# Kernel optimization log

Hardware: AMD Instinct MI355X
Metric: run time of the kernel (lower is better)

Reference implementation:

```python
import jax, jax.numpy as jnp
import numpy as np

B, T, D = 8, 4096, 1024

def setup_inputs() -> dict:
    key = jax.random.key(0)
    k1, k2, k3, k4, k5 = jax.random.split(key, 5)
    s = 1.0 / np.sqrt(D)
    return {
        "seq": jax.random.normal(k1, (B, T, D), dtype=jnp.float32),
        "W_delta": jax.random.uniform(k2, (D, D), jnp.float32, -s, s),
        "b_delta": jax.random.uniform(k3, (D,), jnp.float32, -s, s),
        "W_value": jax.random.uniform(k4, (D, D), jnp.float32, -s, s),
        "b_value": jax.random.uniform(k5, (D,), jnp.float32, -s, s),
    }

def reference(seq, W_delta, b_delta, W_value, b_value):
    # delta = sigmoid(seq @ W_delta^T + b_delta); value = seq @ W_value^T + b_value
    delta = jax.nn.sigmoid(jnp.einsum("btd,ed->bte", seq, W_delta) + b_delta)
    value = jnp.einsum("btd,ed->bte", seq, W_value) + b_value
    # gated linear recurrence: state_t = (1-delta_t)*state_{t-1} + delta_t*value_t
    def step(state, dv):
        d, v = dv  # each [B, D]
        state = (1.0 - d) * state + d * v
        return state, state
    init = jnp.zeros((seq.shape[0], seq.shape[-1]), dtype=seq.dtype)
    # time-major for scan
    _, out = jax.lax.scan(step, init, (delta.transpose(1, 0, 2), value.transpose(1, 0, 2)))
    return out.transpose(1, 0, 2)  # [B, T, D]
```

## Files before the change

kernel.cpp:

```cpp
#include <hip/hip_runtime.h>
#include <hip/hip_bf16.h>


typedef _Float16 f16;
typedef _Float16 f16x8 __attribute__((ext_vector_type(8)));
typedef float    f32x4 __attribute__((ext_vector_type(4)));

#define NB  8
#define NT  4096
#define ND  1024
#define NM  (NB*NT)
#define KK  1024

#define CT  64
#define NCH (NT/CT)

#define OFF_AP     0UL
#define OFF_BP     67108864UL
#define OFF_VALUE  71303168UL
#define OFF_AARR   205520896UL
#define OFF_SARR   207618048UL
#define OFF_SIN    209715200UL

#define GLOAD_LDS16(gp, lp)                                                          \
  __builtin_amdgcn_global_load_lds(                                                  \
      (const __attribute__((address_space(1))) void*)(gp),                           \
      (__attribute__((address_space(3))) void*)(lp), 16, 0, 0)

#define MEMFENCE asm volatile("" ::: "memory")
#define BARRIER() do { MEMFENCE; __builtin_amdgcn_s_barrier(); MEMFENCE; } while (0)
#define WAITV2() asm volatile("s_waitcnt vmcnt(2)" ::: "memory")
#define WAITV0() asm volatile("s_waitcnt vmcnt(0)" ::: "memory")

__global__ void k_convert_seq(const float* __restrict__ src, f16* __restrict__ Ap) {
  const long n8 = (long)NM * ND / 8;
  long i = (long)blockIdx.x * blockDim.x + threadIdx.x;
  const long stride = (long)gridDim.x * blockDim.x;
  for (; i < n8; i += stride) {
    const float4 v0 = *(const float4*)(src + i * 8);
    const float4 v1 = *(const float4*)(src + i * 8 + 4);
    f16x8 h;
    h[0] = (f16)v0.x; h[1] = (f16)v0.y; h[2] = (f16)v0.z; h[3] = (f16)v0.w;
    h[4] = (f16)v1.x; h[5] = (f16)v1.y; h[6] = (f16)v1.z; h[7] = (f16)v1.w;
    *((f16x8*)Ap + i) = h;
  }
}

__global__ void k_convert_w(const float* __restrict__ Wd, const float* __restrict__ Wv,
                            f16* __restrict__ Bp) {
  const long i = (long)blockIdx.x * blockDim.x + threadIdx.x;
  const int n = (int)(i >> 7);
  const int k8 = ((int)i & 127) * 8;
  const float* row = (n < ND) ? (Wd + (long)n * ND) : (Wv + (long)(n - ND) * ND);
  const float4 v0 = *(const float4*)(row + k8);
  const float4 v1 = *(const float4*)(row + k8 + 4);
  f16x8 h;
  h[0] = (f16)v0.x; h[1] = (f16)v0.y; h[2] = (f16)v0.z; h[3] = (f16)v0.w;
  h[4] = (f16)v1.x; h[5] = (f16)v1.y; h[6] = (f16)v1.z; h[7] = (f16)v1.w;
  *(f16x8*)(Bp + (long)n * ND + k8) = h;
}

#define LDS_A(c) ((c) * 65536)
#define LDS_B(c) ((c) * 65536 + 32768)

__global__ __launch_bounds__(512, 2) void k_gemm(
    const f16* __restrict__ Ap, const f16* __restrict__ Bp,
    const float* __restrict__ bd, const float* __restrict__ bv,
    float* __restrict__ dOut, float* __restrict__ vOut) {
  __shared__ char smem[131072];

  const int t = threadIdx.x;
  const int w = t >> 6, lane = t & 63;
  const int wr = w >> 2, wc = w & 3;
  const int l15 = lane & 15, l4 = lane >> 4;

  const int bid = blockIdx.x;
  const int sw = (bid & 7) * 128 + (bid >> 3);
  const int bm = sw >> 3, bn = sw & 7;
  const long m0 = (long)bm * 256;
  const int n0 = bn * 256;

  f32x4 acc[8][4] = {};

  const int rl0 = t >> 3;
  const int rl1 = 64 + (t >> 3);
  const int c16_0 = (t & 7) ^ (rl0 & 7);
  const int c16_1 = (t & 7) ^ (rl1 & 7);

  auto stageA = [&](int kt, int h, int c) {
    const f16* s0 = Ap + (m0 + h * 128 + rl0) * (long)KK + kt * 64 + c16_0 * 8;
    const f16* s1 = Ap + (m0 + h * 128 + rl1) * (long)KK + kt * 64 + c16_1 * 8;
    char* base = smem + LDS_A(c) + h * 16384 + w * 1024;
    GLOAD_LDS16(s0, base);
    GLOAD_LDS16(s1, base + 8192);
  };
  auto stageB = [&](int kt, int h, int c) {
    const f16* s0 = Bp + (long)(n0 + h * 128 + rl0) * ND + kt * 64 + c16_0 * 8;
    const f16* s1 = Bp + (long)(n0 + h * 128 + rl1) * ND + kt * 64 + c16_1 * 8;
    char* base = smem + LDS_B(c) + h * 16384 + w * 1024;
    GLOAD_LDS16(s0, base);
    GLOAD_LDS16(s1, base + 8192);
  };

  f16x8 aF[8], bF[2];
  auto readA = [&](int c, int k) {
#pragma unroll
    for (int mf = 0; mf < 8; ++mf) {
      const int row = wr * 128 + mf * 16 + l15;
      const int c16 = (k * 4 + l4) ^ (row & 7);
      aF[mf] = *(const f16x8*)(smem + LDS_A(c) + row * 128 + c16 * 16);
    }
  };
  auto readB = [&](int c, int k, int nh) {
#pragma unroll
    for (int nfl = 0; nfl < 2; ++nfl) {
      const int row = nh * 128 + wc * 32 + nfl * 16 + l15;
      const int c16 = (k * 4 + l4) ^ (row & 7);
      bF[nfl] = *(const f16x8*)(smem + LDS_B(c) + row * 128 + c16 * 16);
    }
  };
  auto mfmaQ = [&](int nh) {
    __builtin_amdgcn_s_setprio(1);
#pragma unroll
    for (int mf = 0; mf < 8; ++mf)
#pragma unroll
      for (int nfl = 0; nfl < 2; ++nfl)
        acc[mf][nh * 2 + nfl] = __builtin_amdgcn_mfma_f32_16x16x32_f16(
            bF[nfl], aF[mf], acc[mf][nh * 2 + nfl], 0, 0, 0);
    __builtin_amdgcn_s_setprio(0);
  };

  auto tile = [&](int c, int ktNext, bool pf) {
    if (pf) stageA(ktNext, 0, c ^ 1);
    readA(c, 0); readB(c, 0, 0);
    BARRIER();
    mfmaQ(0);
    if (pf) { WAITV2(); } else { WAITV0(); }
    BARRIER();
    if (pf) stageA(ktNext, 1, c ^ 1);
    readB(c, 0, 1);
    BARRIER();
    mfmaQ(1);
    BARRIER();
    if (pf) stageB(ktNext, 0, c ^ 1);
    readA(c, 1); readB(c, 1, 0);
    BARRIER();
    mfmaQ(0);
    BARRIER();
    if (pf) stageB(ktNext, 1, c ^ 1);
    readB(c, 1, 1);
    BARRIER();
    mfmaQ(1);
    if (pf) { WAITV2(); } else { WAITV0(); }
    BARRIER();
  };

  stageA(0, 0, 0); stageA(0, 1, 0); stageB(0, 0, 0); stageB(0, 1, 0);
  WAITV2();
  BARRIER();

  for (int i = 0; i < 8; ++i) {
    tile(0, 2 * i + 1, true);
    tile(1, 2 * i + 2, i < 7);
  }

  const bool isDelta = (n0 < ND);
#pragma unroll
  for (int nf = 0; nf < 4; ++nf) {
    const int nb = n0 + (nf >> 1) * 128 + wc * 32 + (nf & 1) * 16 + l4 * 4;
    const float4 bias = *(const float4*)(isDelta ? (bd + nb) : (bv + (nb - ND)));
#pragma unroll
    for (int mf = 0; mf < 8; ++mf) {
      const long m = m0 + wr * 128 + mf * 16 + l15;
      f32x4 x = acc[mf][nf];
      x[0] += bias.x; x[1] += bias.y; x[2] += bias.z; x[3] += bias.w;
      if (isDelta) {
#pragma unroll
        for (int r = 0; r < 4; ++r) x[r] = 1.0f / (1.0f + __expf(-x[r]));
        *(f32x4*)(dOut + m * ND + nb) = x;
      } else {
        *(f32x4*)(vOut + m * ND + (nb - ND)) = x;
      }
    }
  }
}

__global__ void k_scan_local(const float* __restrict__ delta, const float* __restrict__ value,
                             float* __restrict__ Aarr, float* __restrict__ Sarr) {
  const int bid = blockIdx.x;
  const int c = bid & 63, b = bid >> 6;
  const int d = threadIdx.x * 4;
  const long base = ((long)b * NT + (long)c * CT) * ND + d;
  float4 a = make_float4(1.f, 1.f, 1.f, 1.f);
  float4 s = make_float4(0.f, 0.f, 0.f, 0.f);
#pragma unroll 4
  for (int tt = 0; tt < CT; ++tt) {
    const float4 dl = *(const float4*)(delta + base + (long)tt * ND);
    const float4 v  = *(const float4*)(value + base + (long)tt * ND);
    const float o0 = 1.0f - dl.x, o1 = 1.0f - dl.y, o2 = 1.0f - dl.z, o3 = 1.0f - dl.w;
    a.x *= o0; a.y *= o1; a.z *= o2; a.w *= o3;
    s.x = o0 * s.x + dl.x * v.x;
    s.y = o1 * s.y + dl.y * v.y;
    s.z = o2 * s.z + dl.z * v.z;
    s.w = o3 * s.w + dl.w * v.w;
  }
  const long o = (long)(b * NCH + c) * ND + d;
  *(float4*)(Aarr + o) = a;
  *(float4*)(Sarr + o) = s;
}

__global__ void k_scan_prefix(const float* __restrict__ Aarr, const float* __restrict__ Sarr,
                              float* __restrict__ Sin) {
  const int tid = blockIdx.x * blockDim.x + threadIdx.x;
  const int b = tid >> 8, d = (tid & 255) * 4;
  float4 st = make_float4(0.f, 0.f, 0.f, 0.f);
  for (int c = 0; c < NCH; ++c) {
    const long idx = (long)(b * NCH + c) * ND + d;
    *(float4*)(Sin + idx) = st;
    const float4 a = *(const float4*)(Aarr + idx);
    const float4 s = *(const float4*)(Sarr + idx);
    st.x = a.x * st.x + s.x;
    st.y = a.y * st.y + s.y;
    st.z = a.z * st.z + s.z;
    st.w = a.w * st.w + s.w;
  }
}

__global__ void k_scan_apply(const float* __restrict__ value, const float* __restrict__ Sin,
                             float* __restrict__ out) {
  const int bid = blockIdx.x;
  const int c = bid & 63, b = bid >> 6;
  const int d = threadIdx.x * 4;
  const long base = ((long)b * NT + (long)c * CT) * ND + d;
  float4 st = *(const float4*)(Sin + (long)(b * NCH + c) * ND + d);
#pragma unroll 4
  for (int tt = 0; tt < CT; ++tt) {
    const long idx = base + (long)tt * ND;
    const float4 dl = *(const float4*)(out + idx);
    const float4 v  = *(const float4*)(value + idx);
    st.x = (1.0f - dl.x) * st.x + dl.x * v.x;
    st.y = (1.0f - dl.y) * st.y + dl.y * v.y;
    st.z = (1.0f - dl.z) * st.z + dl.z * v.z;
    st.w = (1.0f - dl.w) * st.w + dl.w * v.w;
    *(float4*)(out + idx) = st;
  }
}

extern "C" void kernel_launch(void* const* d_in, const int* in_sizes, int n_in,
                              void* d_out, int out_size, void* d_ws, size_t ws_size,
                              hipStream_t stream) {
  const float* seq = (const float*)d_in[0];
  const float* Wd  = (const float*)d_in[1];
  const float* bd  = (const float*)d_in[2];
  const float* Wv  = (const float*)d_in[3];
  const float* bv  = (const float*)d_in[4];
  float* out = (float*)d_out;

  char* ws = (char*)d_ws;
  f16*   Ap    = (f16*)(ws + OFF_AP);
  f16*   Bp    = (f16*)(ws + OFF_BP);
  float* value = (float*)(ws + OFF_VALUE);
  float* Aarr  = (float*)(ws + OFF_AARR);
  float* Sarr  = (float*)(ws + OFF_SARR);
  float* Sin   = (float*)(ws + OFF_SIN);

  hipLaunchKernelGGL(k_convert_seq, dim3(2048), dim3(256), 0, stream, seq, Ap);
  hipLaunchKernelGGL(k_convert_w,   dim3(1024), dim3(256), 0, stream, Wd, Wv, Bp);
  hipLaunchKernelGGL(k_gemm, dim3(1024), dim3(512), 0, stream, Ap, Bp, bd, bv, out, value);
  hipLaunchKernelGGL(k_scan_local,  dim3(512), dim3(256), 0, stream, out, value, Aarr, Sarr);
  hipLaunchKernelGGL(k_scan_prefix, dim3(8),   dim3(256), 0, stream, Aarr, Sarr, Sin);
  hipLaunchKernelGGL(k_scan_apply,  dim3(512), dim3(256), 0, stream, value, Sin, out);
}
```

Measured before the change: 519.1 us.

## Store GEMM outputs as fp16 and fuse three-pass scan with lookback flags

The GEMM now writes delta and value as fp16 into workspace instead of fp32, halving the intermediate write and read traffic. The local scan, prefix and apply kernels are merged into one kernel that publishes per-chunk carries behind release flags. Each block then spins on its predecessors' flags and combines their carries serially before its apply pass. This adds fp16 rounding of delta and value and depends on all 512 blocks being co-resident or scheduled in order so the spin-waits do not deadlock.

```diff
diff --git a/kernel.cpp b/kernel.cpp
--- a/kernel.cpp
+++ b/kernel.cpp
@@ -3,6 +3,7 @@
 
 
 typedef _Float16 f16;
+typedef _Float16 f16x4 __attribute__((ext_vector_type(4)));
 typedef _Float16 f16x8 __attribute__((ext_vector_type(8)));
 typedef float    f32x4 __attribute__((ext_vector_type(4)));
 
@@ -17,10 +18,11 @@
 
 #define OFF_AP     0UL
 #define OFF_BP     67108864UL
-#define OFF_VALUE  71303168UL
+#define OFF_DLT    71303168UL
+#define OFF_VAL    138412032UL
 #define OFF_AARR   205520896UL
 #define OFF_SARR   207618048UL
-#define OFF_SIN    209715200UL
+#define OFF_FLAG   209715200UL
 
 #define GLOAD_LDS16(gp, lp)                                                          \
   __builtin_amdgcn_global_load_lds(                                                  \
@@ -31,6 +33,10 @@
 #define BARRIER() do { MEMFENCE; __builtin_amdgcn_s_barrier(); MEMFENCE; } while (0)
 #define WAITV2() asm volatile("s_waitcnt vmcnt(2)" ::: "memory")
 #define WAITV0() asm volatile("s_waitcnt vmcnt(0)" ::: "memory")
+
+__global__ void k_zero_flags(unsigned* __restrict__ flags) {
+  flags[threadIdx.x] = 0u;
+}
 
 __global__ void k_convert_seq(const float* __restrict__ src, f16* __restrict__ Ap) {
   const long n8 = (long)NM * ND / 8;
@@ -66,7 +72,7 @@
 __global__ __launch_bounds__(512, 2) void k_gemm(
     const f16* __restrict__ Ap, const f16* __restrict__ Bp,
     const float* __restrict__ bd, const float* __restrict__ bv,
-    float* __restrict__ dOut, float* __restrict__ vOut) {
+    f16* __restrict__ Dlt, f16* __restrict__ Val) {
   __shared__ char smem[131072];
 
   const int t = threadIdx.x;
@@ -169,6 +175,7 @@
   for (int nf = 0; nf < 4; ++nf) {
     const int nb = n0 + (nf >> 1) * 128 + wc * 32 + (nf & 1) * 16 + l4 * 4;
     const float4 bias = *(const float4*)(isDelta ? (bd + nb) : (bv + (nb - ND)));
+    f16* const dst = isDelta ? (Dlt + nb) : (Val + (nb - ND));
 #pragma unroll
     for (int mf = 0; mf < 8; ++mf) {
       const long m = m0 + wr * 128 + mf * 16 + l15;
@@ -177,71 +184,68 @@
       if (isDelta) {
 #pragma unroll
         for (int r = 0; r < 4; ++r) x[r] = 1.0f / (1.0f + __expf(-x[r]));
-        *(f32x4*)(dOut + m * ND + nb) = x;
-      } else {
-        *(f32x4*)(vOut + m * ND + (nb - ND)) = x;
       }
+      f16x4 h;
+      h[0] = (f16)x[0]; h[1] = (f16)x[1]; h[2] = (f16)x[2]; h[3] = (f16)x[3];
+      *(f16x4*)(dst + m * ND) = h;
     }
   }
 }
 
-__global__ void k_scan_local(const float* __restrict__ delta, const float* __restrict__ value,
-                             float* __restrict__ Aarr, float* __restrict__ Sarr) {
+__global__ __launch_bounds__(256) void k_scan(
+    const f16* __restrict__ Dlt, const f16* __restrict__ Val,
+    float* __restrict__ out, float* __restrict__ Aarr, float* __restrict__ Sarr,
+    unsigned* __restrict__ flags) {
   const int bid = blockIdx.x;
   const int c = bid & 63, b = bid >> 6;
   const int d = threadIdx.x * 4;
   const long base = ((long)b * NT + (long)c * CT) * ND + d;
+
   float4 a = make_float4(1.f, 1.f, 1.f, 1.f);
   float4 s = make_float4(0.f, 0.f, 0.f, 0.f);
 #pragma unroll 4
   for (int tt = 0; tt < CT; ++tt) {
-    const float4 dl = *(const float4*)(delta + base + (long)tt * ND);
-    const float4 v  = *(const float4*)(value + base + (long)tt * ND);
-    const float o0 = 1.0f - dl.x, o1 = 1.0f - dl.y, o2 = 1.0f - dl.z, o3 = 1.0f - dl.w;
+    const f16x4 dh = *(const f16x4*)(Dlt + base + (long)tt * ND);
+    const f16x4 vh = *(const f16x4*)(Val + base + (long)tt * ND);
+    const float d0 = (float)dh[0], d1 = (float)dh[1], d2 = (float)dh[2], d3 = (float)dh[3];
+    const float o0 = 1.f - d0, o1 = 1.f - d1, o2 = 1.f - d2, o3 = 1.f - d3;
     a.x *= o0; a.y *= o1; a.z *= o2; a.w *= o3;
-    s.x = o0 * s.x + dl.x * v.x;
-    s.y = o1 * s.y + dl.y * v.y;
-    s.z = o2 * s.z + dl.z * v.z;
-    s.w = o3 * s.w + dl.w * v.w;
-  }
-  const long o = (long)(b * NCH + c) * ND + d;
+    s.x = o0 * s.x + d0 * (float)vh[0];
+    s.y = o1 * s.y + d1 * (float)vh[1];
+    s.z = o2 * s.z + d2 * (float)vh[2];
+    s.w = o3 * s.w + d3 * (float)vh[3];
+  }
+  const long o = (long)bid * ND + d;
   *(float4*)(Aarr + o) = a;
   *(float4*)(Sarr + o) = s;
-}
-
-__global__ void k_scan_prefix(const float* __restrict__ Aarr, const float* __restrict__ Sarr,
-                              float* __restrict__ Sin) {
-  const int tid = blockIdx.x * blockDim.x + threadIdx.x;
-  const int b = tid >> 8, d = (tid & 255) * 4;
-  float4 st = make_float4(0.f, 0.f, 0.f, 0.f);
-  for (int c = 0; c < NCH; ++c) {
-    const long idx = (long)(b * NCH + c) * ND + d;
-    *(float4*)(Sin + idx) = st;
-    const float4 a = *(const float4*)(Aarr + idx);
-    const float4 s = *(const float4*)(Sarr + idx);
-    st.x = a.x * st.x + s.x;
-    st.y = a.y * st.y + s.y;
-    st.z = a.z * st.z + s.z;
-    st.w = a.w * st.w + s.w;
-  }
-}
-
-__global__ void k_scan_apply(const float* __restrict__ value, const float* __restrict__ Sin,
-                             float* __restrict__ out) {
-  const int bid = blockIdx.x;
-  const int c = bid & 63, b = bid >> 6;
-  const int d = threadIdx.x * 4;
-  const long base = ((long)b * NT + (long)c * CT) * ND + d;
-  float4 st = *(const float4*)(Sin + (long)(b * NCH + c) * ND + d);
+  __syncthreads();
+  __threadfence();
+  if (threadIdx.x == 0)
+    __hip_atomic_store(flags + bid, 1u, __ATOMIC_RELEASE, __HIP_MEMORY_SCOPE_AGENT);
+
+  float4 A = make_float4(1.f, 1.f, 1.f, 1.f);
+  float4 S = make_float4(0.f, 0.f, 0.f, 0.f);
+  for (int p = c - 1; p >= 0; --p) {
+    const unsigned* fp = flags + (b << 6) + p;
+    while (__hip_atomic_load(fp, __ATOMIC_ACQUIRE, __HIP_MEMORY_SCOPE_AGENT) == 0u) {}
+    const long po = (long)((b << 6) + p) * ND + d;
+    const float4 ap = *(const float4*)(Aarr + po);
+    const float4 sp = *(const float4*)(Sarr + po);
+    S.x += A.x * sp.x; S.y += A.y * sp.y; S.z += A.z * sp.z; S.w += A.w * sp.w;
+    A.x *= ap.x; A.y *= ap.y; A.z *= ap.z; A.w *= ap.w;
+  }
+
+  float4 st = S;
 #pragma unroll 4
   for (int tt = 0; tt < CT; ++tt) {
     const long idx = base + (long)tt * ND;
-    const float4 dl = *(const float4*)(out + idx);
-    const float4 v  = *(const float4*)(value + idx);
-    st.x = (1.0f - dl.x) * st.x + dl.x * v.x;
-    st.y = (1.0f - dl.y) * st.y + dl.y * v.y;
-    st.z = (1.0f - dl.z) * st.z + dl.z * v.z;
-    st.w = (1.0f - dl.w) * st.w + dl.w * v.w;
+    const f16x4 dh = *(const f16x4*)(Dlt + idx);
+    const f16x4 vh = *(const f16x4*)(Val + idx);
+    const float d0 = (float)dh[0], d1 = (float)dh[1], d2 = (float)dh[2], d3 = (float)dh[3];
+    st.x = (1.f - d0) * st.x + d0 * (float)vh[0];
+    st.y = (1.f - d1) * st.y + d1 * (float)vh[1];
+    st.z = (1.f - d2) * st.z + d2 * (float)vh[2];
+    st.w = (1.f - d3) * st.w + d3 * (float)vh[3];
     *(float4*)(out + idx) = st;
   }
 }
@@ -257,17 +261,17 @@
   float* out = (float*)d_out;
 
   char* ws = (char*)d_ws;
-  f16*   Ap    = (f16*)(ws + OFF_AP);
-  f16*   Bp    = (f16*)(ws + OFF_BP);
-  float* value = (float*)(ws + OFF_VALUE);
-  float* Aarr  = (float*)(ws + OFF_AARR);
-  float* Sarr  = (float*)(ws + OFF_SARR);
-  float* Sin   = (float*)(ws + OFF_SIN);
-
+  f16*      Ap    = (f16*)(ws + OFF_AP);
+  f16*      Bp    = (f16*)(ws + OFF_BP);
+  f16*      Dlt   = (f16*)(ws + OFF_DLT);
+  f16*      Val   = (f16*)(ws + OFF_VAL);
+  float*    Aarr  = (float*)(ws + OFF_AARR);
+  float*    Sarr  = (float*)(ws + OFF_SARR);
+  unsigned* flags = (unsigned*)(ws + OFF_FLAG);
+
+  hipLaunchKernelGGL(k_zero_flags,  dim3(1),    dim3(512), 0, stream, flags);
   hipLaunchKernelGGL(k_convert_seq, dim3(2048), dim3(256), 0, stream, seq, Ap);
   hipLaunchKernelGGL(k_convert_w,   dim3(1024), dim3(256), 0, stream, Wd, Wv, Bp);
-  hipLaunchKernelGGL(k_gemm, dim3(1024), dim3(512), 0, stream, Ap, Bp, bd, bv, out, value);
-  hipLaunchKernelGGL(k_scan_local,  dim3(512), dim3(256), 0, stream, out, value, Aarr, Sarr);
-  hipLaunchKernelGGL(k_scan_prefix, dim3(8),   dim3(256), 0, stream, Aarr, Sarr, Sin);
-  hipLaunchKernelGGL(k_scan_apply,  dim3(512), dim3(256), 0, stream, value, Sin, out);
-}
+  hipLaunchKernelGGL(k_gemm, dim3(1024), dim3(512), 0, stream, Ap, Bp, bd, bv, Dlt, Val);
+  hipLaunchKernelGGL(k_scan, dim3(512), dim3(256), 0, stream, Dlt, Val, out, Aarr, Sarr, flags);
+}
```

New measurement: 970.4 us. 86.9% more time.
